# Kernel tuning notes

Measured on AMD Instinct MI355X. Metric: run time of the kernel, lower is better.

The kernel has to match this reference:

```python
import jax, jax.numpy as jnp
import numpy as np

N = 100000          # num nodes
E = 1600000         # num edges
EMB = 192           # embedding_dimension (divisible by 3)
THIRD = EMB // 3    # 64
NUM_REL = 2
SLOPE = 0.01        # LeakyReLU default negative slope


def leaky_relu(x):
    return jnp.where(x >= 0, x, SLOPE * x)


def setup_inputs() -> dict:
    key = jax.random.key(0)
    ks = jax.random.split(key, 20)
    s = 0.02
    inp = {
        "des": jax.random.normal(ks[0], (N, 768), jnp.float32),
        "tweet": jax.random.normal(ks[1], (N, 768), jnp.float32),
        "num_prop": jax.random.normal(ks[2], (N, 4), jnp.float32),
        "cat_prop": jax.random.normal(ks[3], (N, 3), jnp.float32),
        "edge_index": jax.random.randint(ks[4], (2, E), 0, N, jnp.int64).astype(jnp.int32),
        "edge_type": jax.random.randint(ks[5], (E,), 0, NUM_REL, jnp.int32),
        # params
        "W_des": s * jax.random.normal(ks[6], (768, THIRD), jnp.float32),
        "b_des": jnp.zeros((THIRD,), jnp.float32),
        "W_num": s * jax.random.normal(ks[7], (4, THIRD), jnp.float32),
        "b_num": jnp.zeros((THIRD,), jnp.float32),
        "W_cat": s * jax.random.normal(ks[8], (3, THIRD), jnp.float32),
        "b_cat": jnp.zeros((THIRD,), jnp.float32),
        "W_in": s * jax.random.normal(ks[9], (EMB, EMB), jnp.float32),
        "b_in": jnp.zeros((EMB,), jnp.float32),
        "W_root": s * jax.random.normal(ks[10], (EMB, EMB), jnp.float32),
        "W_rel": s * jax.random.normal(ks[11], (NUM_REL, EMB, EMB), jnp.float32),
        "b_rgcn": jnp.zeros((EMB,), jnp.float32),
        "W_o1": s * jax.random.normal(ks[12], (EMB, EMB), jnp.float32),
        "b_o1": jnp.zeros((EMB,), jnp.float32),
        "W_o2": s * jax.random.normal(ks[13], (EMB, 2), jnp.float32),
        "b_o2": jnp.zeros((2,), jnp.float32),
    }
    return inp


def rgcn_conv(x, edge_index, edge_type, W_root, W_rel, b_rgcn):
    # PyG RGCNConv (default): out = x @ W_root + b + sum_r mean_{edges r -> i}(x[src] @ W_r)
    # mean of (x_j @ W_r) == (mean of x_j) @ W_r, so aggregate first (cheaper).
    src, dst = edge_index[0], edge_index[1]
    h = x[src]  # [E, EMB] gather
    out = x @ W_root + b_rgcn
    for r in range(NUM_REL):
        m = (edge_type == r).astype(x.dtype)  # [E]
        s = jax.ops.segment_sum(h * m[:, None], dst, num_segments=N)  # [N, EMB]
        cnt = jax.ops.segment_sum(m, dst, num_segments=N)             # [N]
        agg = s / jnp.maximum(cnt, 1.0)[:, None]
        out = out + agg @ W_rel[r]
    return out


def reference(des, tweet, num_prop, cat_prop, edge_index, edge_type,
              W_des, b_des, W_num, b_num, W_cat, b_cat, W_in, b_in,
              W_root, W_rel, b_rgcn, W_o1, b_o1, W_o2, b_o2):
    d = leaky_relu(des @ W_des + b_des)
    n = leaky_relu(num_prop @ W_num + b_num)
    c = leaky_relu(cat_prop @ W_cat + b_cat)
    x = jnp.concatenate((d, n, c), axis=1)          # [N, EMB]
    x = leaky_relu(x @ W_in + b_in)
    x = rgcn_conv(x, edge_index, edge_type, W_root, W_rel, b_rgcn)
    # dropout in eval mode = identity
    x = rgcn_conv(x, edge_index, edge_type, W_root, W_rel, b_rgcn)
    x = leaky_relu(x @ W_o1 + b_o1)
    x = x @ W_o2 + b_o2                              # [N, 2]
    return x
```

## Files before the change

### kernel.cpp

```cpp
#include <hip/hip_runtime.h>

typedef _Float16 f16;
typedef _Float16 f16x4 __attribute__((ext_vector_type(4)));
typedef _Float16 f16x8 __attribute__((ext_vector_type(8)));
typedef float f32x4 __attribute__((ext_vector_type(4)));

#define LRELU(v) ((v) >= 0.f ? (v) : 0.01f * (v))

__device__ __forceinline__ int swz(int a) { return a ^ (((a >> 7) & 7) << 4); }

__device__ __forceinline__ f16x4 shflx4(f16x4 v, int m) {
  union { f16x4 h; int i[2]; } u;
  u.h = v;
  u.i[0] = __shfl_xor(u.i[0], m);
  u.i[1] = __shfl_xor(u.i[1], m);
  return u.h;
}

#define TILE 4096

__global__ __launch_bounds__(256) void setup_kernel(
    const float* __restrict__ num_prop, const float* __restrict__ cat_prop,
    const float* __restrict__ W_num, const float* __restrict__ b_num,
    const float* __restrict__ W_cat, const float* __restrict__ b_cat,
    const float* __restrict__ W_des, const float* __restrict__ W_in,
    const float* __restrict__ W_root, const float* __restrict__ W_rel,
    const float* __restrict__ W_o1,
    f16* __restrict__ x0,
    f16* __restrict__ WtDes, f16* __restrict__ WtIn, f16* __restrict__ WtR,
    f16* __restrict__ WtO1,
    const int* __restrict__ ei, int* __restrict__ hist,
    int N, int nbf, int E, int NB)
{
  __shared__ int h[512];
  int b = blockIdx.x;
  int tid = threadIdx.x;
  if (b < nbf) {
    int w = (b * 256 + tid) >> 6;
    int lane = tid & 63;
    if (w < N) {
      const float* npr = num_prop + (size_t)w * 4;
      const float* cpr = cat_prop + (size_t)w * 3;
      float vn = b_num[lane];
#pragma unroll
      for (int k = 0; k < 4; k++) vn += npr[k] * W_num[k * 64 + lane];
      float vc = b_cat[lane];
#pragma unroll
      for (int k = 0; k < 3; k++) vc += cpr[k] * W_cat[k * 64 + lane];
      vn = LRELU(vn);
      vc = LRELU(vc);
      x0[(size_t)w * 192 + 64 + lane] = (f16)vn;
      x0[(size_t)w * 192 + 128 + lane] = (f16)vc;
    }
    return;
  }
  b -= nbf;
  if (b < 192) {
    int idx = b * 256 + tid;
    if (idx < 64 * 768) { int n = idx / 768, k = idx % 768; WtDes[idx] = (f16)W_des[k * 64 + n]; }
    return;
  }
  b -= 192;
  if (b < 144) {
    int idx = b * 256 + tid;
    if (idx < 192 * 192) { int n = idx / 192, k = idx % 192; WtIn[idx] = (f16)W_in[k * 192 + n]; }
    return;
  }
  b -= 144;
  if (b < 432) {
    int idx = b * 256 + tid;
    if (idx < 192 * 576) {
      int n = idx / 576, k = idx % 576;
      int seg = k / 192, kk = k % 192;
      float v = (seg == 0) ? W_root[kk * 192 + n] : W_rel[(seg - 1) * 192 * 192 + kk * 192 + n];
      WtR[idx] = (f16)v;
    }
    return;
  }
  b -= 432;
  if (b < 144) {
    int idx = b * 256 + tid;
    if (idx < 192 * 192) { int n = idx / 192, k = idx % 192; WtO1[idx] = (f16)W_o1[k * 192 + n]; }
    return;
  }
  b -= 144;
  for (int i = tid; i < NB; i += 256) h[i] = 0;
  __syncthreads();
  const int base = b * TILE;
#pragma unroll
  for (int i = 0; i < TILE / 256; ++i) {
    int e = base + i * 256 + tid;
    if (e < E) atomicAdd(&h[ei[E + e] >> 8], 1);
  }
  __syncthreads();
  for (int i = tid; i < NB; i += 256) hist[b * NB + i] = h[i];
}

__global__ __launch_bounds__(512) void scan_kernel(
    int* __restrict__ hist, int* __restrict__ binbase, int NB, int NBLK)
{
  __shared__ int s[512];
  const int b = threadIdx.x;
  int total = 0;
  if (b < NB) {
#pragma unroll 8
    for (int blk = 0; blk < NBLK; ++blk) total += hist[blk * NB + b];
  }
  s[b] = total;
  __syncthreads();
  for (int off = 1; off < 512; off <<= 1) {
    int v = (b >= off) ? s[b - off] : 0;
    __syncthreads();
    s[b] += v;
    __syncthreads();
  }
  int ex = (b == 0) ? 0 : s[b - 1];
  if (b < NB) binbase[b] = ex;
  if (b == 0) binbase[NB] = s[511];
  if (b < NB) {
    int run = ex;
#pragma unroll 8
    for (int blk = 0; blk < NBLK; ++blk) {
      int t = hist[blk * NB + b];
      hist[blk * NB + b] = run;
      run += t;
    }
  }
}

__global__ __launch_bounds__(256) void scatterdes_kernel(
    const float* __restrict__ A, const f16* __restrict__ Bt,
    const float* __restrict__ bias, f16* __restrict__ C, int M,
    const int* __restrict__ ei, const int* __restrict__ et,
    const int* __restrict__ hist, int* __restrict__ sorted,
    int E, int NB, int nbDES)
{
  __shared__ f16 lA[128 * 64];
  __shared__ f16 lB[64 * 64];
  const int tid = threadIdx.x;
  if ((int)blockIdx.x >= nbDES) {
    int blk = (int)blockIdx.x - nbDES;
    int* cur = (int*)lA;
    for (int i = tid; i < NB; i += 256) cur[i] = hist[blk * NB + i];
    __syncthreads();
    const int base = blk * TILE;
#pragma unroll
    for (int i = 0; i < TILE / 256; ++i) {
      int e = base + i * 256 + tid;
      if (e < E) {
        int src = ei[e];
        int dst = ei[E + e];
        int r = et[e];
        int slot = atomicAdd(&cur[dst >> 8], 1);
        sorted[slot] = src | (r << 17) | ((dst & 255) << 18);
      }
    }
    return;
  }
  const int lane = tid & 63, wid = tid >> 6;
  const int wm = wid >> 1, wn = wid & 1;
  const int m0 = blockIdx.x * 128;
  f32x4 acc[4][2] = {};
  const int arow = tid >> 1, ahalf = tid & 1;
  int agr = m0 + arow;
  if (agr >= M) agr = M - 1;
  const float* asrc = A + (size_t)agr * 768 + ahalf * 32;
  for (int k0 = 0; k0 < 768; k0 += 64) {
    {
      const float4* s4 = reinterpret_cast<const float4*>(asrc + k0);
#pragma unroll
      for (int i = 0; i < 4; i++) {
        float4 u = s4[2 * i], w = s4[2 * i + 1];
        f16x8 h;
        h[0] = (f16)u.x; h[1] = (f16)u.y; h[2] = (f16)u.z; h[3] = (f16)u.w;
        h[4] = (f16)w.x; h[5] = (f16)w.y; h[6] = (f16)w.z; h[7] = (f16)w.w;
        int boff = arow * 128 + ahalf * 64 + i * 16;
        *reinterpret_cast<f16x8*>((char*)lA + swz(boff)) = h;
      }
    }
    {
#pragma unroll
      for (int i = 0; i < 2; i++) {
        int c = tid + i * 256;
        int n = c >> 3, k8 = c & 7;
        f16x8 h = *reinterpret_cast<const f16x8*>(Bt + (size_t)n * 768 + k0 + k8 * 8);
        *reinterpret_cast<f16x8*>((char*)lB + swz(n * 128 + k8 * 16)) = h;
      }
    }
    __syncthreads();
#pragma unroll
    for (int ks = 0; ks < 2; ks++) {
      f16x8 af[4], bf[2];
#pragma unroll
      for (int fm = 0; fm < 4; fm++) {
        int row = wm * 64 + fm * 16 + (lane & 15);
        af[fm] = *reinterpret_cast<const f16x8*>((const char*)lA + swz(row * 128 + ks * 64 + (lane >> 4) * 16));
      }
#pragma unroll
      for (int fn = 0; fn < 2; fn++) {
        int nn = wn * 32 + fn * 16 + (lane & 15);
        bf[fn] = *reinterpret_cast<const f16x8*>((const char*)lB + swz(nn * 128 + ks * 64 + (lane >> 4) * 16));
      }
#pragma unroll
      for (int fm = 0; fm < 4; fm++)
#pragma unroll
        for (int fn = 0; fn < 2; fn++)
          acc[fm][fn] = __builtin_amdgcn_mfma_f32_16x16x32_f16(af[fm], bf[fn], acc[fm][fn], 0, 0, 0);
    }
    __syncthreads();
  }
#pragma unroll
  for (int fm = 0; fm < 4; fm++) {
#pragma unroll
    for (int fn = 0; fn < 2; fn++) {
      int gc = wn * 32 + fn * 16 + (lane & 15);
      float b = bias[gc];
#pragma unroll
      for (int r = 0; r < 4; r++) {
        int gr = m0 + wm * 64 + fm * 16 + (lane >> 4) * 4 + r;
        if (gr < M) {
          float v = acc[fm][fn][r] + b;
          C[(size_t)gr * 192 + gc] = (f16)LRELU(v);
        }
      }
    }
  }
}

template <int NSEG, bool RELU, bool OUT2, bool BUILD>
__global__ __launch_bounds__(512) void gemm_x_kernel(
    const f16* __restrict__ A0, const f16* __restrict__ A1, const f16* __restrict__ A2,
    const f16* __restrict__ Bt, const float* __restrict__ bias,
    f16* __restrict__ C, int M,
    const float* __restrict__ W_o2, const float* __restrict__ b_o2,
    float* __restrict__ out,
    const int* __restrict__ sorted, const int* __restrict__ binbase,
    int* __restrict__ csr, int* __restrict__ rowptr, int nbGEMM)
{
  __shared__ f16 lA[128 * 64];
  __shared__ f16 lB[192 * 64];
  const int tid = threadIdx.x;
  if (BUILD && (int)blockIdx.x >= nbGEMM) {
    int bb = (int)blockIdx.x - nbGEMM;
    int* dcount = (int*)lA;
    int* lbase  = dcount + 256;
    int* cur    = lbase + 256;
    if (tid < 256) { dcount[tid] = 0; cur[tid] = 0; }
    __syncthreads();
    int start = binbase[bb], end = binbase[bb + 1];
    for (int j = start + tid; j < end; j += 512)
      atomicAdd(&dcount[(sorted[j] >> 18) & 255], 1);
    __syncthreads();
    if (tid < 256) lbase[tid] = dcount[tid];
    __syncthreads();
    for (int off = 1; off < 256; off <<= 1) {
      int v = 0;
      if (tid < 256 && tid >= off) v = lbase[tid - off];
      __syncthreads();
      if (tid < 256) lbase[tid] += v;
      __syncthreads();
    }
    if (tid < 256) {
      int dst = (bb << 8) + tid;
      if (dst < M) rowptr[dst] = start + lbase[tid] - dcount[tid];
    }
    __syncthreads();
    for (int j = start + tid; j < end; j += 512) {
      int it = sorted[j];
      int dl = (it >> 18) & 255;
      int pos = atomicAdd(&cur[dl], 1);
      int exb = start + lbase[dl] - dcount[dl];
      csr[exb + pos] = (it & 0x1FFFF) | (int)(((unsigned)((it >> 17) & 1)) << 31);
    }
    return;
  }
  const int lane = tid & 63, wid = tid >> 6;
  const int wm = wid >> 2, wn = wid & 3;
  const int m0 = blockIdx.x * 128;
  const int Ktot = NSEG * 192;
  f32x4 acc[4][3] = {};
  const f16* segs[3] = {A0, A1, A2};
  const int arow = tid >> 2, aq = tid & 3;
  int agr = m0 + arow;
  if (agr >= M) agr = M - 1;
  int seg = 0, kin = 0;
  for (int it = 0; it < NSEG * 3; it++) {
    {
      const f16x8* s8 = reinterpret_cast<const f16x8*>(segs[seg] + (size_t)agr * 192 + kin + aq * 16);
      f16x8 h0 = s8[0], h1 = s8[1];
      int b0 = arow * 128 + aq * 32;
      *reinterpret_cast<f16x8*>((char*)lA + swz(b0)) = h0;
      *reinterpret_cast<f16x8*>((char*)lA + swz(b0 + 16)) = h1;
    }
    {
      int kb = it * 64;
#pragma unroll
      for (int i = 0; i < 3; i++) {
        int c = tid + i * 512;
        int n = c >> 3, k8 = c & 7;
        f16x8 h = *reinterpret_cast<const f16x8*>(Bt + (size_t)n * Ktot + kb + k8 * 8);
        *reinterpret_cast<f16x8*>((char*)lB + swz(n * 128 + k8 * 16)) = h;
      }
    }
    __syncthreads();
#pragma unroll
    for (int ks = 0; ks < 2; ks++) {
      f16x8 af[4], bf[3];
#pragma unroll
      for (int fm = 0; fm < 4; fm++) {
        int row = wm * 64 + fm * 16 + (lane & 15);
        af[fm] = *reinterpret_cast<const f16x8*>((const char*)lA + swz(row * 128 + ks * 64 + (lane >> 4) * 16));
      }
#pragma unroll
      for (int fn = 0; fn < 3; fn++) {
        int nn = wn * 48 + fn * 16 + (lane & 15);
        bf[fn] = *reinterpret_cast<const f16x8*>((const char*)lB + swz(nn * 128 + ks * 64 + (lane >> 4) * 16));
      }
#pragma unroll
      for (int fm = 0; fm < 4; fm++)
#pragma unroll
        for (int fn = 0; fn < 3; fn++)
          acc[fm][fn] = __builtin_amdgcn_mfma_f32_16x16x32_f16(af[fm], bf[fn], acc[fm][fn], 0, 0, 0);
    }
    __syncthreads();
    kin += 64;
    if (kin == 192) { kin = 0; if (seg < NSEG - 1) seg++; }
  }
  if (OUT2) {
    __shared__ float red[128][2];
    for (int i = tid; i < 256; i += 512) ((float*)red)[i] = 0.f;
    __syncthreads();
    float bb2[3], w2v[3][2];
#pragma unroll
    for (int fn = 0; fn < 3; fn++) {
      int gc = wn * 48 + fn * 16 + (lane & 15);
      bb2[fn] = bias[gc];
      w2v[fn][0] = W_o2[gc * 2 + 0];
      w2v[fn][1] = W_o2[gc * 2 + 1];
    }
#pragma unroll
    for (int fm = 0; fm < 4; fm++) {
#pragma unroll
      for (int r = 0; r < 4; r++) {
        float p0 = 0.f, p1 = 0.f;
#pragma unroll
        for (int fn = 0; fn < 3; fn++) {
          float v = acc[fm][fn][r] + bb2[fn];
          v = LRELU(v);
          p0 += v * w2v[fn][0];
          p1 += v * w2v[fn][1];
        }
#pragma unroll
        for (int m = 1; m < 16; m <<= 1) { p0 += __shfl_xor(p0, m); p1 += __shfl_xor(p1, m); }
        if ((lane & 15) == 0) {
          int lr = wm * 64 + fm * 16 + (lane >> 4) * 4 + r;
          atomicAdd(&red[lr][0], p0);
          atomicAdd(&red[lr][1], p1);
        }
      }
    }
    __syncthreads();
    if (tid < 256) {
      int gr = m0 + (tid >> 1);
      if (gr < M) out[(size_t)gr * 2 + (tid & 1)] = red[tid >> 1][tid & 1] + b_o2[tid & 1];
    }
  } else {
#pragma unroll
    for (int fm = 0; fm < 4; fm++) {
#pragma unroll
      for (int fn = 0; fn < 3; fn++) {
        int gc = wn * 48 + fn * 16 + (lane & 15);
        float b = bias[gc];
#pragma unroll
        for (int r = 0; r < 4; r++) {
          int gr = m0 + wm * 64 + fm * 16 + (lane >> 4) * 4 + r;
          if (gr < M) {
            float v = acc[fm][fn][r] + b;
            if (RELU) v = LRELU(v);
            C[(size_t)gr * 192 + gc] = (f16)v;
          }
        }
      }
    }
  }
}

__global__ __launch_bounds__(256) void agg_kernel(
    const f16* __restrict__ x, const int* __restrict__ csr,
    const int* __restrict__ rowptr,
    f16* __restrict__ agg0, f16* __restrict__ agg1, int N, int Etot)
{
  int w = (blockIdx.x << 2) + (threadIdx.x >> 6);
  if (w >= N) return;
  const int lane = threadIdx.x & 63;
  const int g = lane >> 4, sub = lane & 15;
  int start = rowptr[w];
  int end = (w == N - 1) ? Etot : rowptr[w + 1];
  int deg = end - start;
  f16x4 a0[3] = {}, a1[3] = {};
  float c1f = 0.f;
  int nj = (deg + 15) >> 4;
  for (int j = 0; j < nj; ++j) {
    int base = start + j * 16 + g * 4;
#pragma unroll
    for (int i = 0; i < 4; ++i) {
      int idx = j * 16 + g * 4 + i;
      if (idx < deg) {
        int e = csr[base + i];
        int src = e & 0x7fffffff;
        const f16* rowp = x + (size_t)src * 192 + sub * 4;
        f16x4 v0 = *reinterpret_cast<const f16x4*>(rowp);
        f16x4 v1 = *reinterpret_cast<const f16x4*>(rowp + 64);
        f16x4 v2 = *reinterpret_cast<const f16x4*>(rowp + 128);
        if (e < 0) {
          c1f += 1.f;
          a1[0] += v0; a1[1] += v1; a1[2] += v2;
        } else {
          a0[0] += v0; a0[1] += v1; a0[2] += v2;
        }
      }
    }
  }
#pragma unroll
  for (int c = 0; c < 3; ++c) {
    a0[c] += shflx4(a0[c], 16); a0[c] += shflx4(a0[c], 32);
    a1[c] += shflx4(a1[c], 16); a1[c] += shflx4(a1[c], 32);
  }
  c1f += __shfl_xor(c1f, 16); c1f += __shfl_xor(c1f, 32);
  if (g == 0) {
    float c0f = (float)deg - c1f;
    float i0 = 1.f / fmaxf(c0f, 1.f);
    float i1 = 1.f / fmaxf(c1f, 1.f);
#pragma unroll
    for (int c = 0; c < 3; ++c) {
      f16x4 o0, o1;
#pragma unroll
      for (int k = 0; k < 4; ++k) {
        o0[k] = (f16)((float)a0[c][k] * i0);
        o1[k] = (f16)((float)a1[c][k] * i1);
      }
      *reinterpret_cast<f16x4*>(agg0 + (size_t)w * 192 + c * 64 + sub * 4) = o0;
      *reinterpret_cast<f16x4*>(agg1 + (size_t)w * 192 + c * 64 + sub * 4) = o1;
    }
  }
}

extern "C" void kernel_launch(void* const* d_in, const int* in_sizes, int n_in,
                              void* d_out, int out_size, void* d_ws, size_t ws_size,
                              hipStream_t stream)
{
  const float* des      = (const float*)d_in[0];
  const float* num_prop = (const float*)d_in[2];
  const float* cat_prop = (const float*)d_in[3];
  const int* edge_index = (const int*)d_in[4];
  const int* edge_type  = (const int*)d_in[5];
  const float* W_des = (const float*)d_in[6];
  const float* b_des = (const float*)d_in[7];
  const float* W_num = (const float*)d_in[8];
  const float* b_num = (const float*)d_in[9];
  const float* W_cat = (const float*)d_in[10];
  const float* b_cat = (const float*)d_in[11];
  const float* W_in  = (const float*)d_in[12];
  const float* b_in  = (const float*)d_in[13];
  const float* W_root= (const float*)d_in[14];
  const float* W_rel = (const float*)d_in[15];
  const float* b_rgcn= (const float*)d_in[16];
  const float* W_o1  = (const float*)d_in[17];
  const float* b_o1  = (const float*)d_in[18];
  const float* W_o2  = (const float*)d_in[19];
  const float* b_o2  = (const float*)d_in[20];
  float* out = (float*)d_out;

  const int N = in_sizes[2] / 4;
  const int E = in_sizes[5];
  (void)n_in; (void)out_size; (void)ws_size;

  const int NB = (N + 255) >> 8;
  const int NBLK = (E + TILE - 1) / TILE;

  char* base = (char*)d_ws;
  size_t off = 0;
  auto take = [&](size_t bytes) -> void* {
    void* p = base + off;
    off += (bytes + 255) & ~(size_t)255;
    return p;
  };
  f16* xA      = (f16*)take((size_t)N * 192 * 2);
  f16* xB      = (f16*)take((size_t)N * 192 * 2);
  f16* agg0    = (f16*)take((size_t)N * 192 * 2);
  f16* agg1    = (f16*)take((size_t)N * 192 * 2);
  int* sorted  = (int*)take((size_t)E * 4);
  int* csr     = (int*)take((size_t)E * 4);
  int* rowptr  = (int*)take((size_t)(N + 4) * 4);
  int* hist    = (int*)take((size_t)NBLK * NB * 4);
  int* binbase = (int*)take((size_t)(NB + 2) * 4);
  f16* WtDes   = (f16*)take(64 * 768 * 2);
  f16* WtIn    = (f16*)take(192 * 192 * 2);
  f16* WtR     = (f16*)take(192 * 576 * 2);
  f16* WtO1    = (f16*)take(192 * 192 * 2);

  const int nbf = (N + 3) / 4;
  const int nsetup = nbf + 192 + 144 + 432 + 144 + NBLK;
  setup_kernel<<<nsetup, 256, 0, stream>>>(
      num_prop, cat_prop, W_num, b_num, W_cat, b_cat,
      W_des, W_in, W_root, W_rel, W_o1,
      xA, WtDes, WtIn, WtR, WtO1,
      edge_index, hist, N, nbf, E, NB);
  scan_kernel<<<1, 512, 0, stream>>>(hist, binbase, NB, NBLK);
  const int nbDES = (N + 127) / 128;
  scatterdes_kernel<<<nbDES + NBLK, 256, 0, stream>>>(
      des, WtDes, b_des, xA, N, edge_index, edge_type, hist, sorted, E, NB, nbDES);
  const int nbX = (N + 127) / 128;
  gemm_x_kernel<1, true, false, true><<<nbX + NB, 512, 0, stream>>>(
      xA, xA, xA, WtIn, b_in, xB, N, nullptr, nullptr, nullptr,
      sorted, binbase, csr, rowptr, nbX);
  agg_kernel<<<(N + 3) / 4, 256, 0, stream>>>(xB, csr, rowptr, agg0, agg1, N, E);
  gemm_x_kernel<3, false, false, false><<<nbX, 512, 0, stream>>>(
      xB, agg0, agg1, WtR, b_rgcn, xA, N, nullptr, nullptr, nullptr,
      nullptr, nullptr, nullptr, nullptr, nbX);
  agg_kernel<<<(N + 3) / 4, 256, 0, stream>>>(xA, csr, rowptr, agg0, agg1, N, E);
  gemm_x_kernel<3, false, false, false><<<nbX, 512, 0, stream>>>(
      xA, agg0, agg1, WtR, b_rgcn, xB, N, nullptr, nullptr, nullptr,
      nullptr, nullptr, nullptr, nullptr, nbX);
  gemm_x_kernel<1, false, true, false><<<nbX, 512, 0, stream>>>(
      xB, xB, xB, WtO1, b_o1, nullptr, N, W_o2, b_o2, out,
      nullptr, nullptr, nullptr, nullptr, nbX);
}
```

Measured before the change: 529.2 us.

## Drop LDS staging in GEMMs; load MFMA fragments directly from global memory

```diff
diff --git a/kernel.cpp b/kernel.cpp
--- a/kernel.cpp
+++ b/kernel.cpp
@@ -6,8 +6,6 @@
 typedef float f32x4 __attribute__((ext_vector_type(4)));
 
 #define LRELU(v) ((v) >= 0.f ? (v) : 0.01f * (v))
-
-__device__ __forceinline__ int swz(int a) { return a ^ (((a >> 7) & 7) << 4); }
 
 __device__ __forceinline__ f16x4 shflx4(f16x4 v, int m) {
   union { f16x4 h; int i[2]; } u;
@@ -135,13 +133,11 @@
     const int* __restrict__ hist, int* __restrict__ sorted,
     int E, int NB, int nbDES)
 {
-  __shared__ f16 lA[128 * 64];
-  __shared__ f16 lB[64 * 64];
+  __shared__ int scur[512];
   const int tid = threadIdx.x;
   if ((int)blockIdx.x >= nbDES) {
     int blk = (int)blockIdx.x - nbDES;
-    int* cur = (int*)lA;
-    for (int i = tid; i < NB; i += 256) cur[i] = hist[blk * NB + i];
+    for (int i = tid; i < NB; i += 256) scur[i] = hist[blk * NB + i];
     __syncthreads();
     const int base = blk * TILE;
 #pragma unroll
@@ -151,7 +147,7 @@
         int src = ei[e];
         int dst = ei[E + e];
         int r = et[e];
-        int slot = atomicAdd(&cur[dst >> 8], 1);
+        int slot = atomicAdd(&scur[dst >> 8], 1);
         sorted[slot] = src | (r << 17) | ((dst & 255) << 18);
       }
     }
@@ -160,64 +156,74 @@
   const int lane = tid & 63, wid = tid >> 6;
   const int wm = wid >> 1, wn = wid & 1;
   const int m0 = blockIdx.x * 128;
+  const int l15 = lane & 15, lhi = lane >> 4;
   f32x4 acc[4][2] = {};
-  const int arow = tid >> 1, ahalf = tid & 1;
-  int agr = m0 + arow;
-  if (agr >= M) agr = M - 1;
-  const float* asrc = A + (size_t)agr * 768 + ahalf * 32;
-  for (int k0 = 0; k0 < 768; k0 += 64) {
-    {
-      const float4* s4 = reinterpret_cast<const float4*>(asrc + k0);
-#pragma unroll
-      for (int i = 0; i < 4; i++) {
-        float4 u = s4[2 * i], w = s4[2 * i + 1];
-        f16x8 h;
-        h[0] = (f16)u.x; h[1] = (f16)u.y; h[2] = (f16)u.z; h[3] = (f16)u.w;
-        h[4] = (f16)w.x; h[5] = (f16)w.y; h[6] = (f16)w.z; h[7] = (f16)w.w;
-        int boff = arow * 128 + ahalf * 64 + i * 16;
-        *reinterpret_cast<f16x8*>((char*)lA + swz(boff)) = h;
-      }
-    }
-    {
-#pragma unroll
-      for (int i = 0; i < 2; i++) {
-        int c = tid + i * 256;
-        int n = c >> 3, k8 = c & 7;
-        f16x8 h = *reinterpret_cast<const f16x8*>(Bt + (size_t)n * 768 + k0 + k8 * 8);
-        *reinterpret_cast<f16x8*>((char*)lB + swz(n * 128 + k8 * 16)) = h;
-      }
-    }
-    __syncthreads();
-#pragma unroll
-    for (int ks = 0; ks < 2; ks++) {
-      f16x8 af[4], bf[2];
-#pragma unroll
-      for (int fm = 0; fm < 4; fm++) {
-        int row = wm * 64 + fm * 16 + (lane & 15);
-        af[fm] = *reinterpret_cast<const f16x8*>((const char*)lA + swz(row * 128 + ks * 64 + (lane >> 4) * 16));
-      }
-#pragma unroll
-      for (int fn = 0; fn < 2; fn++) {
-        int nn = wn * 32 + fn * 16 + (lane & 15);
-        bf[fn] = *reinterpret_cast<const f16x8*>((const char*)lB + swz(nn * 128 + ks * 64 + (lane >> 4) * 16));
-      }
-#pragma unroll
-      for (int fm = 0; fm < 4; fm++)
-#pragma unroll
-        for (int fn = 0; fn < 2; fn++)
-          acc[fm][fn] = __builtin_amdgcn_mfma_f32_16x16x32_f16(af[fm], bf[fn], acc[fm][fn], 0, 0, 0);
-    }
-    __syncthreads();
+  const float* aB[4];
+#pragma unroll
+  for (int fm = 0; fm < 4; ++fm) {
+    int gr = m0 + wm * 64 + fm * 16 + l15;
+    if (gr >= M) gr = M - 1;
+    aB[fm] = A + (size_t)gr * 768 + lhi * 8;
+  }
+  const f16* bB[2];
+#pragma unroll
+  for (int fn = 0; fn < 2; ++fn)
+    bB[fn] = Bt + (size_t)(wn * 32 + fn * 16 + l15) * 768 + lhi * 8;
+
+  float4 ac[4][2];
+  f16x8 bc[2];
+#pragma unroll
+  for (int fm = 0; fm < 4; ++fm) {
+    const float4* p = reinterpret_cast<const float4*>(aB[fm]);
+    ac[fm][0] = p[0]; ac[fm][1] = p[1];
+  }
+#pragma unroll
+  for (int fn = 0; fn < 2; ++fn)
+    bc[fn] = *reinterpret_cast<const f16x8*>(bB[fn]);
+
+#pragma unroll 4
+  for (int k0 = 0; k0 < 768; k0 += 32) {
+    float4 an[4][2];
+    f16x8 bn[2];
+    if (k0 + 32 < 768) {
+#pragma unroll
+      for (int fm = 0; fm < 4; ++fm) {
+        const float4* p = reinterpret_cast<const float4*>(aB[fm] + k0 + 32);
+        an[fm][0] = p[0]; an[fm][1] = p[1];
+      }
+#pragma unroll
+      for (int fn = 0; fn < 2; ++fn)
+        bn[fn] = *reinterpret_cast<const f16x8*>(bB[fn] + k0 + 32);
+    }
+    f16x8 af[4];
+#pragma unroll
+    for (int fm = 0; fm < 4; ++fm) {
+      af[fm][0] = (f16)ac[fm][0].x; af[fm][1] = (f16)ac[fm][0].y;
+      af[fm][2] = (f16)ac[fm][0].z; af[fm][3] = (f16)ac[fm][0].w;
+      af[fm][4] = (f16)ac[fm][1].x; af[fm][5] = (f16)ac[fm][1].y;
+      af[fm][6] = (f16)ac[fm][1].z; af[fm][7] = (f16)ac[fm][1].w;
+    }
+#pragma unroll
+    for (int fm = 0; fm < 4; ++fm)
+#pragma unroll
+      for (int fn = 0; fn < 2; ++fn)
+        acc[fm][fn] = __builtin_amdgcn_mfma_f32_16x16x32_f16(af[fm], bc[fn], acc[fm][fn], 0, 0, 0);
+    if (k0 + 32 < 768) {
+#pragma unroll
+      for (int fm = 0; fm < 4; ++fm) { ac[fm][0] = an[fm][0]; ac[fm][1] = an[fm][1]; }
+#pragma unroll
+      for (int fn = 0; fn < 2; ++fn) bc[fn] = bn[fn];
+    }
   }
 #pragma unroll
   for (int fm = 0; fm < 4; fm++) {
 #pragma unroll
     for (int fn = 0; fn < 2; fn++) {
-      int gc = wn * 32 + fn * 16 + (lane & 15);
+      int gc = wn * 32 + fn * 16 + l15;
       float b = bias[gc];
 #pragma unroll
       for (int r = 0; r < 4; r++) {
-        int gr = m0 + wm * 64 + fm * 16 + (lane >> 4) * 4 + r;
+        int gr = m0 + wm * 64 + fm * 16 + lhi * 4 + r;
         if (gr < M) {
           float v = acc[fm][fn][r] + b;
           C[(size_t)gr * 192 + gc] = (f16)LRELU(v);
@@ -228,7 +234,7 @@
 }
 
 template <int NSEG, bool RELU, bool OUT2, bool BUILD>
-__global__ __launch_bounds__(512) void gemm_x_kernel(
+__global__ __launch_bounds__(256) void gemm_x_kernel(
     const f16* __restrict__ A0, const f16* __restrict__ A1, const f16* __restrict__ A2,
     const f16* __restrict__ Bt, const float* __restrict__ bias,
     f16* __restrict__ C, int M,
@@ -237,35 +243,34 @@
     const int* __restrict__ sorted, const int* __restrict__ binbase,
     int* __restrict__ csr, int* __restrict__ rowptr, int nbGEMM)
 {
-  __shared__ f16 lA[128 * 64];
-  __shared__ f16 lB[192 * 64];
+  __shared__ int smem_i[768];
+  __shared__ float red[64][2];
   const int tid = threadIdx.x;
   if (BUILD && (int)blockIdx.x >= nbGEMM) {
     int bb = (int)blockIdx.x - nbGEMM;
-    int* dcount = (int*)lA;
-    int* lbase  = dcount + 256;
-    int* cur    = lbase + 256;
-    if (tid < 256) { dcount[tid] = 0; cur[tid] = 0; }
+    int* dcount = smem_i;
+    int* lbase  = smem_i + 256;
+    int* cur    = smem_i + 512;
+    dcount[tid] = 0; cur[tid] = 0;
     __syncthreads();
     int start = binbase[bb], end = binbase[bb + 1];
-    for (int j = start + tid; j < end; j += 512)
+    for (int j = start + tid; j < end; j += 256)
       atomicAdd(&dcount[(sorted[j] >> 18) & 255], 1);
     __syncthreads();
-    if (tid < 256) lbase[tid] = dcount[tid];
+    lbase[tid] = dcount[tid];
     __syncthreads();
     for (int off = 1; off < 256; off <<= 1) {
-      int v = 0;
-      if (tid < 256 && tid >= off) v = lbase[tid - off];
+      int v = (tid >= off) ? lbase[tid - off] : 0;
       __syncthreads();
-      if (tid < 256) lbase[tid] += v;
+      lbase[tid] += v;
       __syncthreads();
     }
-    if (tid < 256) {
+    {
       int dst = (bb << 8) + tid;
       if (dst < M) rowptr[dst] = start + lbase[tid] - dcount[tid];
     }
     __syncthreads();
-    for (int j = start + tid; j < end; j += 512) {
+    for (int j = start + tid; j < end; j += 256) {
       int it = sorted[j];
       int dl = (it >> 18) & 255;
       int pos = atomicAdd(&cur[dl], 1);
@@ -274,66 +279,54 @@
     }
     return;
   }
-  const int lane = tid & 63, wid = tid >> 6;
-  const int wm = wid >> 2, wn = wid & 3;
-  const int m0 = blockIdx.x * 128;
+  const int lane = tid & 63, wn = tid >> 6;
+  const int l15 = lane & 15, lhi = lane >> 4;
+  const int m0 = blockIdx.x * 64;
   const int Ktot = NSEG * 192;
   f32x4 acc[4][3] = {};
   const f16* segs[3] = {A0, A1, A2};
-  const int arow = tid >> 2, aq = tid & 3;
-  int agr = m0 + arow;
-  if (agr >= M) agr = M - 1;
-  int seg = 0, kin = 0;
-  for (int it = 0; it < NSEG * 3; it++) {
-    {
-      const f16x8* s8 = reinterpret_cast<const f16x8*>(segs[seg] + (size_t)agr * 192 + kin + aq * 16);
-      f16x8 h0 = s8[0], h1 = s8[1];
-      int b0 = arow * 128 + aq * 32;
-      *reinterpret_cast<f16x8*>((char*)lA + swz(b0)) = h0;
-      *reinterpret_cast<f16x8*>((char*)lA + swz(b0 + 16)) = h1;
-    }
-    {
-      int kb = it * 64;
-#pragma unroll
-      for (int i = 0; i < 3; i++) {
-        int c = tid + i * 512;
-        int n = c >> 3, k8 = c & 7;
-        f16x8 h = *reinterpret_cast<const f16x8*>(Bt + (size_t)n * Ktot + kb + k8 * 8);
-        *reinterpret_cast<f16x8*>((char*)lB + swz(n * 128 + k8 * 16)) = h;
-      }
-    }
-    __syncthreads();
-#pragma unroll
-    for (int ks = 0; ks < 2; ks++) {
+  int gro[4];
+#pragma unroll
+  for (int fm = 0; fm < 4; ++fm) {
+    int gr = m0 + fm * 16 + l15;
+    if (gr >= M) gr = M - 1;
+    gro[fm] = gr;
+  }
+  const f16* bB[3];
+#pragma unroll
+  for (int fn = 0; fn < 3; ++fn)
+    bB[fn] = Bt + (size_t)(wn * 48 + fn * 16 + l15) * Ktot + lhi * 8;
+
+#pragma unroll
+  for (int seg = 0; seg < NSEG; ++seg) {
+    const f16* As = segs[seg];
+    const f16* aP[4];
+#pragma unroll
+    for (int fm = 0; fm < 4; ++fm)
+      aP[fm] = As + (size_t)gro[fm] * 192 + lhi * 8;
+#pragma unroll
+    for (int c = 0; c < 6; ++c) {
       f16x8 af[4], bf[3];
 #pragma unroll
-      for (int fm = 0; fm < 4; fm++) {
-        int row = wm * 64 + fm * 16 + (lane & 15);
-        af[fm] = *reinterpret_cast<const f16x8*>((const char*)lA + swz(row * 128 + ks * 64 + (lane >> 4) * 16));
-      }
-#pragma unroll
-      for (int fn = 0; fn < 3; fn++) {
-        int nn = wn * 48 + fn * 16 + (lane & 15);
-        bf[fn] = *reinterpret_cast<const f16x8*>((const char*)lB + swz(nn * 128 + ks * 64 + (lane >> 4) * 16));
-      }
-#pragma unroll
-      for (int fm = 0; fm < 4; fm++)
-#pragma unroll
-        for (int fn = 0; fn < 3; fn++)
+      for (int fm = 0; fm < 4; ++fm)
+        af[fm] = *reinterpret_cast<const f16x8*>(aP[fm] + c * 32);
+#pragma unroll
+      for (int fn = 0; fn < 3; ++fn)
+        bf[fn] = *reinterpret_cast<const f16x8*>(bB[fn] + seg * 192 + c * 32);
+#pragma unroll
+      for (int fm = 0; fm < 4; ++fm)
+#pragma unroll
+        for (int fn = 0; fn < 3; ++fn)
           acc[fm][fn] = __builtin_amdgcn_mfma_f32_16x16x32_f16(af[fm], bf[fn], acc[fm][fn], 0, 0, 0);
     }
-    __syncthreads();
-    kin += 64;
-    if (kin == 192) { kin = 0; if (seg < NSEG - 1) seg++; }
   }
   if (OUT2) {
-    __shared__ float red[128][2];
-    for (int i = tid; i < 256; i += 512) ((float*)red)[i] = 0.f;
+    if (tid < 128) ((float*)red)[tid] = 0.f;
     __syncthreads();
     float bb2[3], w2v[3][2];
 #pragma unroll
     for (int fn = 0; fn < 3; fn++) {
-      int gc = wn * 48 + fn * 16 + (lane & 15);
+      int gc = wn * 48 + fn * 16 + l15;
       bb2[fn] = bias[gc];
       w2v[fn][0] = W_o2[gc * 2 + 0];
       w2v[fn][1] = W_o2[gc * 2 + 1];
@@ -352,15 +345,15 @@
         }
 #pragma unroll
         for (int m = 1; m < 16; m <<= 1) { p0 += __shfl_xor(p0, m); p1 += __shfl_xor(p1, m); }
-        if ((lane & 15) == 0) {
-          int lr = wm * 64 + fm * 16 + (lane >> 4) * 4 + r;
+        if (l15 == 0) {
+          int lr = fm * 16 + lhi * 4 + r;
           atomicAdd(&red[lr][0], p0);
           atomicAdd(&red[lr][1], p1);
         }
       }
     }
     __syncthreads();
-    if (tid < 256) {
+    if (tid < 128) {
       int gr = m0 + (tid >> 1);
       if (gr < M) out[(size_t)gr * 2 + (tid & 1)] = red[tid >> 1][tid & 1] + b_o2[tid & 1];
     }
@@ -369,11 +362,11 @@
     for (int fm = 0; fm < 4; fm++) {
 #pragma unroll
       for (int fn = 0; fn < 3; fn++) {
-        int gc = wn * 48 + fn * 16 + (lane & 15);
+        int gc = wn * 48 + fn * 16 + l15;
         float b = bias[gc];
 #pragma unroll
         for (int r = 0; r < 4; r++) {
-          int gr = m0 + wm * 64 + fm * 16 + (lane >> 4) * 4 + r;
+          int gr = m0 + fm * 16 + lhi * 4 + r;
           if (gr < M) {
             float v = acc[fm][fn][r] + b;
             if (RELU) v = LRELU(v);
@@ -510,19 +503,19 @@
   const int nbDES = (N + 127) / 128;
   scatterdes_kernel<<<nbDES + NBLK, 256, 0, stream>>>(
       des, WtDes, b_des, xA, N, edge_index, edge_type, hist, sorted, E, NB, nbDES);
-  const int nbX = (N + 127) / 128;
-  gemm_x_kernel<1, true, false, true><<<nbX + NB, 512, 0, stream>>>(
+  const int nbX = (N + 63) / 64;
+  gemm_x_kernel<1, true, false, true><<<nbX + NB, 256, 0, stream>>>(
       xA, xA, xA, WtIn, b_in, xB, N, nullptr, nullptr, nullptr,
       sorted, binbase, csr, rowptr, nbX);
   agg_kernel<<<(N + 3) / 4, 256, 0, stream>>>(xB, csr, rowptr, agg0, agg1, N, E);
-  gemm_x_kernel<3, false, false, false><<<nbX, 512, 0, stream>>>(
+  gemm_x_kernel<3, false, false, false><<<nbX, 256, 0, stream>>>(
       xB, agg0, agg1, WtR, b_rgcn, xA, N, nullptr, nullptr, nullptr,
       nullptr, nullptr, nullptr, nullptr, nbX);
   agg_kernel<<<(N + 3) / 4, 256, 0, stream>>>(xA, csr, rowptr, agg0, agg1, N, E);
-  gemm_x_kernel<3, false, false, false><<<nbX, 512, 0, stream>>>(
+  gemm_x_kernel<3, false, false, false><<<nbX, 256, 0, stream>>>(
       xA, agg0, agg1, WtR, b_rgcn, xB, N, nullptr, nullptr, nullptr,
       nullptr, nullptr, nullptr, nullptr, nbX);
-  gemm_x_kernel<1, false, true, false><<<nbX, 512, 0, stream>>>(
+  gemm_x_kernel<1, false, true, false><<<nbX, 256, 0, stream>>>(
       xB, xB, xB, WtO1, b_o1, nullptr, N, W_o2, b_o2, out,
       nullptr, nullptr, nullptr, nullptr, nbX);
 }
```

Result: slower. 713.5 us (+34.8%).
